# Optimization experiments

Measured on AMD Instinct MI355X. Metric: run time of the kernel, lower is better.

Reference implementation:

```python
import jax, jax.numpy as jnp
import numpy as np

MEL = 80  # seq2seq_dim


def gru_step(x, h, Wg, bg, Wc, bc):
    """TF GRUCell: gates=[r,u], new_h = u*h + (1-u)*c."""
    gates = jax.nn.sigmoid(jnp.concatenate([x, h], axis=-1) @ Wg + bg)
    r, u = jnp.split(gates, 2, axis=-1)
    c = jnp.tanh(jnp.concatenate([x, r * h], axis=-1) @ Wc + bc)
    return u * h + (1.0 - u) * c


def setup_inputs() -> dict:
    key = jax.random.key(0)
    B, T_enc, D_enc = 128, 1024, 256
    n_styles, style_dim = 10, 256
    reduc, T_dec = 5, 250
    ks = jax.random.split(key, 20)
    rn = lambda k, shape, s=0.05: jax.random.normal(k, shape, jnp.float32) * s
    return {
        "encoder_output": rn(ks[0], (B, T_enc, D_enc), 1.0),
        "inp_mask": jax.random.randint(ks[1], (B,), 1, T_enc + 1, dtype=jnp.int32),
        "inp_att": jax.nn.softmax(rn(ks[2], (B, n_styles), 1.0), axis=-1),
        "style_token": rn(ks[3], (n_styles, style_dim)),
        # decoder prenet 80->256->128
        "pre_W1": rn(ks[4], (MEL, 256)), "pre_b1": jnp.zeros((256,), jnp.float32),
        "pre_W2": rn(ks[5], (256, 128)), "pre_b2": jnp.zeros((128,), jnp.float32),
        # attention GRU cell: input = [context(256), prenet(128)] = 384, hidden 256
        "att_Wg": rn(ks[6], (384 + 256, 512)), "att_bg": jnp.ones((512,), jnp.float32),
        "att_Wc": rn(ks[7], (384 + 256, 256)), "att_bc": jnp.zeros((256,), jnp.float32),
        # Bahdanau attention (depth 256)
        "attn_Wk": rn(ks[8], (256, 256)), "attn_bk": jnp.zeros((256,), jnp.float32),
        "attn_Wq": rn(ks[9], (256, 256)), "attn_bq": jnp.zeros((256,), jnp.float32),
        "attn_v": rn(ks[10], (256,)),
        # dec_input dense: [att_out(256), weighting_context(256)] -> 256
        "deci_W": rn(ks[11], (512, 256)), "deci_b": jnp.zeros((256,), jnp.float32),
        # two residual GRU decoder layers (hidden 256)
        "dec1_Wg": rn(ks[12], (512, 512)), "dec1_bg": jnp.ones((512,), jnp.float32),
        "dec1_Wc": rn(ks[13], (512, 256)), "dec1_bc": jnp.zeros((256,), jnp.float32),
        "dec2_Wg": rn(ks[14], (512, 512)), "dec2_bg": jnp.ones((512,), jnp.float32),
        "dec2_Wc": rn(ks[15], (512, 256)), "dec2_bc": jnp.zeros((256,), jnp.float32),
        # output projection 256 -> mel*reduc
        "out_W": rn(ks[16], (256, MEL * reduc)), "out_b": jnp.zeros((MEL * reduc,), jnp.float32),
        "decode_time_steps": T_dec,
    }


def reference(encoder_output, inp_mask, inp_att, style_token,
              pre_W1, pre_b1, pre_W2, pre_b2,
              att_Wg, att_bg, att_Wc, att_bc,
              attn_Wk, attn_bk, attn_Wq, attn_bq, attn_v,
              deci_W, deci_b,
              dec1_Wg, dec1_bg, dec1_Wc, dec1_bc,
              dec2_Wg, dec2_bg, dec2_Wc, dec2_bc,
              out_W, out_b, decode_time_steps):
    B, T_enc, D = encoder_output.shape
    reduc = out_W.shape[1] // MEL
    # precompute attention keys and mask (done once in TF AttentionModule)
    keys = encoder_output @ attn_Wk + attn_bk                       # [B, T_enc, 256]
    mask = jnp.arange(T_enc)[None, :] < inp_mask[:, None]           # [B, T_enc]
    sentence_style = inp_att @ style_token                          # [B, 256]
    abs_style = jnp.abs(sentence_style)

    carry0 = (
        jnp.zeros((B, 256), jnp.float32),   # att GRU state
        jnp.zeros((B, 256), jnp.float32),   # dec GRU layer 1 state
        jnp.zeros((B, 256), jnp.float32),   # dec GRU layer 2 state
        jnp.zeros((B, 256), jnp.float32),   # last context
        jnp.zeros((B, MEL), jnp.float32),   # go frame / last output
    )

    def step(carry, _):
        h_att, h1, h2, ctx, last_out = carry
        # decoder prenet (dropout inactive, training=False)
        p = jax.nn.relu(last_out @ pre_W1 + pre_b1)
        p = jax.nn.relu(p @ pre_W2 + pre_b2)
        # attention RNN
        h_att = gru_step(jnp.concatenate([ctx, p], axis=-1), h_att,
                         att_Wg, att_bg, att_Wc, att_bc)
        # Bahdanau attention with query = attention cell state
        q = h_att @ attn_Wq + attn_bq                               # [B, 256]
        e = jnp.einsum('btd,d->bt', jnp.tanh(keys + q[:, None, :]), attn_v)
        e = jnp.where(mask, e, -1e9)
        alpha = jax.nn.softmax(e, axis=-1)                          # [B, T_enc]
        context = jnp.einsum('bt,btd->bd', alpha, encoder_output)   # [B, 256]
        # style-weighted context
        wctx = context + sentence_style
        weight_per = jnp.mean(abs_style / (jnp.abs(context) + abs_style))
        # decoder RNN: dense then 2 residual GRU layers
        dec_in = jnp.concatenate([h_att, wctx], axis=-1) @ deci_W + deci_b
        h1 = gru_step(dec_in, h1, dec1_Wg, dec1_bg, dec1_Wc, dec1_bc)
        o1 = h1 + dec_in
        h2 = gru_step(o1, h2, dec2_Wg, dec2_bg, dec2_Wc, dec2_bc)
        o2 = h2 + o1
        dense_out = o2 @ out_W + out_b                              # [B, mel*reduc]
        new_out = dense_out[:, -MEL:]
        return (h_att, h1, h2, context, new_out), (dense_out, alpha, weight_per)

    _, (dense_outs, alphas, weight_pers) = jax.lax.scan(
        step, carry0, None, length=decode_time_steps)
    # [T_dec, B, mel*reduc] -> [B, T_dec*reduc, mel]
    seq2seq_output = jnp.transpose(dense_outs, (1, 0, 2)).reshape(
        B, decode_time_steps * reduc, MEL)
    return seq2seq_output, alphas, weight_pers
```

## Files before the change

kernel.cpp:

```cpp
#include <hip/hip_runtime.h>
#include <cstdint>
#include <cstddef>


#define TDEC   250
#define BATCH  128

#define ALPHA_OFF  ((size_t)12800000)
#define WP_OFF     ((size_t)45568000)

#define WS_WACC_B   ((size_t)0)
#define WS_WGT_B    ((size_t)4096)
#define WGT_ELEMS   1658880
#define WS_KEYS_B   (WS_WGT_B + (size_t)WGT_ELEMS * 2)
#define WS_ENC_B    (WS_KEYS_B + (size_t)33554432 * 2)

#define OFF_PRE_W1   0
#define OFF_PRE_W2   20480
#define OFF_ATT_WG   53248
#define OFF_ATT_WC   380928
#define OFF_ATT_WCH  479232
#define OFF_ATTN_WQ  544768
#define OFF_DECI_W   610304
#define OFF_DEC1_WG  741376
#define OFF_DEC1_WC  1003520
#define OFF_DEC1_WCH 1069056
#define OFF_DEC2_WG  1134592
#define OFF_DEC2_WC  1396736
#define OFF_DEC2_WCH 1462272
#define OFF_OUT_WP   1527808

__device__ inline float bf2f(unsigned short u){
    return __uint_as_float(((unsigned int)u) << 16);
}
__device__ inline unsigned short f2bf(float f){
    unsigned int u = __float_as_uint(f);
    u = (u + 0x7fffu + ((u >> 16) & 1u)) >> 16;
    return (unsigned short)u;
}
__device__ inline float ftanh(float x){
    float e = __expf(2.f * x);
    return 1.f - 2.f * __builtin_amdgcn_rcpf(e + 1.f);
}
__device__ inline float fsig(float x){
    return __builtin_amdgcn_rcpf(1.f + __expf(-x));
}

template<int K, int N, int PARTS>
__device__ inline void gemv_part(const unsigned short* __restrict__ W,
                                 const float* __restrict__ x,
                                 float* __restrict__ scratch, int tid)
{
    constexpr int CH   = N / 8;
    constexpr int LG   = (CH == 16) ? 4 : (CH == 32) ? 5 : 6;
    constexpr int KCNT = K / PARTS;
    static_assert(KCNT * PARTS == K, "K must divide");
    static_assert(CH * PARTS <= 1024, "too many threads");
    const int chunk = tid & (CH - 1);
    const int part  = tid >> LG;
    if (PARTS == (1024 >> LG) || part < PARTS){
        const uint4* Wp = (const uint4*)W + (size_t)(part * KCNT) * (N / 8) + chunk;
        const float* xp = x + part * KCNT;
        float a0=0.f,a1=0.f,a2=0.f,a3=0.f,a4=0.f,a5=0.f,a6=0.f,a7=0.f;
        #pragma unroll 8
        for (int k = 0; k < KCNT; k++){
            uint4 w = Wp[(size_t)k * (N / 8)];
            float xv = xp[k];
            a0 = fmaf(__uint_as_float(w.x << 16),         xv, a0);
            a1 = fmaf(__uint_as_float(w.x & 0xffff0000u), xv, a1);
            a2 = fmaf(__uint_as_float(w.y << 16),         xv, a2);
            a3 = fmaf(__uint_as_float(w.y & 0xffff0000u), xv, a3);
            a4 = fmaf(__uint_as_float(w.z << 16),         xv, a4);
            a5 = fmaf(__uint_as_float(w.z & 0xffff0000u), xv, a5);
            a6 = fmaf(__uint_as_float(w.w << 16),         xv, a6);
            a7 = fmaf(__uint_as_float(w.w & 0xffff0000u), xv, a7);
        }
        float4* s4 = (float4*)(scratch + part * N + chunk * 8);
        s4[0] = float4{a0, a1, a2, a3};
        s4[1] = float4{a4, a5, a6, a7};
    }
}

template<int N, int PARTS>
__device__ inline float red_parts(const float* __restrict__ scratch, int n){
    float s = 0.f;
    #pragma unroll
    for (int p = 0; p < PARTS; p++) s += scratch[p * N + n];
    return s;
}

__global__ void k_cvt_flat(const float* __restrict__ src, unsigned short* __restrict__ dst, int n){
    int i = blockIdx.x * 256 + threadIdx.x;
    if (i < n) dst[i] = f2bf(src[i]);
}
__global__ void k_cvt_pad(const float* __restrict__ src, unsigned short* __restrict__ dst){
    int i = blockIdx.x * 256 + threadIdx.x;
    int k = i >> 9, n = i & 511;
    dst[i] = (n < 400) ? f2bf(src[k * 400 + n]) : (unsigned short)0;
}

__global__ __launch_bounds__(256) void k_keys(const float* __restrict__ enc,
                                              const float* __restrict__ Wk,
                                              const float* __restrict__ bk,
                                              unsigned short* __restrict__ keysT)
{
    __shared__ __align__(16) float Wt[64 * 256];
    __shared__ float At[64 * 64];
    __shared__ unsigned short tileT[256 * 68];
    const int tid = threadIdx.x;
    const size_t row0 = (size_t)blockIdx.x * 64;
    const int dq = tid & 63;
    const int rg = tid >> 6;

    float4 acc[16];
    #pragma unroll
    for (int i = 0; i < 16; i++) acc[i] = float4{0.f, 0.f, 0.f, 0.f};

    for (int k0 = 0; k0 < 256; k0 += 64){
        __syncthreads();
        #pragma unroll
        for (int i = 0; i < 64; i++)
            Wt[i * 256 + tid] = Wk[(size_t)(k0 + i) * 256 + tid];
        #pragma unroll
        for (int i = 0; i < 16; i++){
            int idx = tid + i * 256;
            int r = idx >> 6, kk = idx & 63;
            At[idx] = enc[(row0 + r) * 256 + k0 + kk];
        }
        __syncthreads();
        for (int kk = 0; kk < 64; kk++){
            float4 w = ((const float4*)Wt)[kk * 64 + dq];
            #pragma unroll
            for (int rr = 0; rr < 16; rr++){
                float a = At[(rg * 16 + rr) * 64 + kk];
                acc[rr].x += a * w.x; acc[rr].y += a * w.y;
                acc[rr].z += a * w.z; acc[rr].w += a * w.w;
            }
        }
    }
    float4 bb = ((const float4*)bk)[dq];
    __syncthreads();
    #pragma unroll
    for (int rr = 0; rr < 16; rr++){
        int t_loc = rg * 16 + rr;
        #pragma unroll
        for (int c = 0; c < 4; c++){
            float val = (&acc[rr].x)[c] + (&bb.x)[c];
            int d = dq * 4 + c;
            tileT[d * 68 + t_loc] = f2bf(val);
        }
    }
    __syncthreads();
    const int b_ = (int)(row0 >> 10);
    const int t0 = (int)(row0 & 1023);
    #pragma unroll
    for (int i = 0; i < 16; i++){
        int flat = tid + i * 256;
        int d = flat >> 4, tq = flat & 15;
        ushort4 v = *(const ushort4*)&tileT[d * 68 + tq * 4];
        *(ushort4*)&keysT[(((size_t)(b_ * 256 + d)) << 10) + t0 + tq * 4] = v;
    }
}

struct KParams {
    const int *imask; const float *inp_att; const float *style_tok;
    const float *pre_b1, *pre_b2, *att_bg, *att_bc, *attn_bq, *attn_v;
    const float *deci_b, *dec1_bg, *dec1_bc, *dec2_bg, *dec2_bc, *out_b;
    const unsigned short *wgt;
    const unsigned short *keysT;
    const unsigned short *encb;
    float *wacc; float *out;
};

__global__ __launch_bounds__(1024, 1) void k_main(KParams p)
{
    __shared__ __align__(16) float scr [8192];
    __shared__ __align__(16) float scr2[8192];
    __shared__ float xa[640];
    __shared__ float xg[512];
    __shared__ float xr[256];
    __shared__ float xd[512];
    __shared__ float g_l[512], cx_l[256];
    __shared__ float h_att[256], h1[256], h2[256];
    __shared__ float p1_l[256], dci[256], o1_l[256], o2_l[256];
    __shared__ float stylel[256], astylel[256], v_l[256], q_l[256];
    __shared__ float e_l[1024];
    __shared__ float last_o[80];
    __shared__ float red[16];

    const int tid = threadIdx.x;
    const int b   = blockIdx.x;
    const int mlen = p.imask[b];
    const unsigned short* W = p.wgt;

    if (tid < 256){
        h_att[tid] = 0.f; h1[tid] = 0.f; h2[tid] = 0.f;
        float s = 0.f;
        #pragma unroll
        for (int k = 0; k < 10; k++) s += p.inp_att[b * 10 + k] * p.style_tok[k * 256 + tid];
        stylel[tid] = s; astylel[tid] = fabsf(s);
        v_l[tid] = p.attn_v[tid];
        xa[tid] = 0.f;
        xa[384 + tid] = 0.f;
    }
    if (tid < 80) last_o[tid] = 0.f;
    __syncthreads();

    for (int s = 0; s < TDEC; s++){
        gemv_part<80, 256, 16>(W + OFF_PRE_W1, last_o, scr, tid);
        __syncthreads();
        if (tid < 256)
            p1_l[tid] = fmaxf(p.pre_b1[tid] + red_parts<256,16>(scr, tid), 0.f);
        __syncthreads();

        gemv_part<256, 128, 64>(W + OFF_PRE_W2, p1_l, scr, tid);
        __syncthreads();
        if (tid < 128)
            xa[256 + tid] = fmaxf(p.pre_b2[tid] + red_parts<128,64>(scr, tid), 0.f);
        __syncthreads();

        gemv_part<640, 512, 16>(W + OFF_ATT_WG, xa, scr,  tid);
        gemv_part<384, 256, 32>(W + OFF_ATT_WC, xa, scr2, tid);
        __syncthreads();
        if (tid < 512){
            float g = fsig(p.att_bg[tid] + red_parts<512,16>(scr, tid));
            g_l[tid] = g;
            if (tid < 256) xr[tid] = g * h_att[tid];
        } else if (tid < 768){
            int n = tid - 512;
            cx_l[n] = p.att_bc[n] + red_parts<256,32>(scr2, n);
        }
        __syncthreads();

        gemv_part<256, 256, 32>(W + OFF_ATT_WCH, xr, scr, tid);
        __syncthreads();
        if (tid < 256){
            float c = ftanh(cx_l[tid] + red_parts<256,32>(scr, tid));
            float u = g_l[256 + tid];
            float h = u * h_att[tid] + (1.f - u) * c;
            h_att[tid] = h;
            xa[384 + tid] = h;
            xd[tid] = h;
        }
        __syncthreads();

        gemv_part<256, 256, 32>(W + OFF_ATTN_WQ, h_att, scr, tid);
        __syncthreads();
        if (tid < 256) q_l[tid] = p.attn_bq[tid] + red_parts<256,32>(scr, tid);
        __syncthreads();

        {
            const int tc   = tid & 127;
            const int part = tid >> 7;
            float acc0=0.f,acc1=0.f,acc2=0.f,acc3=0.f,acc4=0.f,acc5=0.f,acc6=0.f,acc7=0.f;
            if (tc * 8 < mlen){
                const unsigned short* kp = p.keysT + (((size_t)b) << 18)
                                         + ((size_t)(part * 32) << 10) + tc * 8;
                #pragma unroll 16
                for (int dd = 0; dd < 32; dd++){
                    uint4 kv = *(const uint4*)(kp + ((size_t)dd << 10));
                    int d = part * 32 + dd;
                    float qd = q_l[d], vd = v_l[d];
                    acc0 = fmaf(ftanh(__uint_as_float(kv.x << 16)         + qd), vd, acc0);
                    acc1 = fmaf(ftanh(__uint_as_float(kv.x & 0xffff0000u) + qd), vd, acc1);
                    acc2 = fmaf(ftanh(__uint_as_float(kv.y << 16)         + qd), vd, acc2);
                    acc3 = fmaf(ftanh(__uint_as_float(kv.y & 0xffff0000u) + qd), vd, acc3);
                    acc4 = fmaf(ftanh(__uint_as_float(kv.z << 16)         + qd), vd, acc4);
                    acc5 = fmaf(ftanh(__uint_as_float(kv.z & 0xffff0000u) + qd), vd, acc5);
                    acc6 = fmaf(ftanh(__uint_as_float(kv.w << 16)         + qd), vd, acc6);
                    acc7 = fmaf(ftanh(__uint_as_float(kv.w & 0xffff0000u) + qd), vd, acc7);
                }
            }
            float4* s4 = (float4*)(scr + part * 1024 + tc * 8);
            s4[0] = float4{acc0, acc1, acc2, acc3};
            s4[1] = float4{acc4, acc5, acc6, acc7};
        }
        __syncthreads();
        float av = 0.f;
        if (tid < mlen){
            float s8 = 0.f;
            #pragma unroll
            for (int pp = 0; pp < 8; pp++) s8 += scr[pp * 1024 + tid];
            av = __expf(s8);
        }
        {
            float ws = av;
            #pragma unroll
            for (int off = 32; off; off >>= 1) ws += __shfl_xor(ws, off, 64);
            if ((tid & 63) == 0) red[tid >> 6] = ws;
        }
        __syncthreads();
        {
            float tot = 0.f;
            #pragma unroll
            for (int i = 0; i < 16; i++) tot += red[i];
            float alpha = av * __builtin_amdgcn_rcpf(tot);
            e_l[tid] = alpha;
            __builtin_nontemporal_store(alpha,
                &p.out[ALPHA_OFF + (size_t)s * 131072 + ((size_t)b << 10) + tid]);
        }
        __syncthreads();

        {
            const int dc = tid & 31;
            const int tp = tid >> 5;
            float acc0=0.f,acc1=0.f,acc2=0.f,acc3=0.f,acc4=0.f,acc5=0.f,acc6=0.f,acc7=0.f;
            const unsigned short* er = p.encb + (((size_t)b) << 18) + dc * 8;
            #pragma unroll 8
            for (int t = tp; t < mlen; t += 32){
                uint4 ev4 = *(const uint4*)(er + ((size_t)t << 8));
                float al = e_l[t];
                acc0 = fmaf(al, __uint_as_float(ev4.x << 16),         acc0);
                acc1 = fmaf(al, __uint_as_float(ev4.x & 0xffff0000u), acc1);
                acc2 = fmaf(al, __uint_as_float(ev4.y << 16),         acc2);
                acc3 = fmaf(al, __uint_as_float(ev4.y & 0xffff0000u), acc3);
                acc4 = fmaf(al, __uint_as_float(ev4.z << 16),         acc4);
                acc5 = fmaf(al, __uint_as_float(ev4.z & 0xffff0000u), acc5);
                acc6 = fmaf(al, __uint_as_float(ev4.w << 16),         acc6);
                acc7 = fmaf(al, __uint_as_float(ev4.w & 0xffff0000u), acc7);
            }
            float4* s4 = (float4*)(scr + tp * 256 + dc * 8);
            s4[0] = float4{acc0, acc1, acc2, acc3};
            s4[1] = float4{acc4, acc5, acc6, acc7};
        }
        __syncthreads();
        if (tid < 256){
            float cs = red_parts<256,32>(scr, tid);
            xa[tid] = cs;
            xd[256 + tid] = cs + stylel[tid];
            float wpv = astylel[tid] * __builtin_amdgcn_rcpf(fabsf(cs) + astylel[tid]);
            #pragma unroll
            for (int off = 32; off; off >>= 1) wpv += __shfl_xor(wpv, off, 64);
            if ((tid & 63) == 0) atomicAdd(&p.wacc[s], wpv);
        }
        __syncthreads();

        gemv_part<512, 256, 32>(W + OFF_DECI_W, xd, scr, tid);
        __syncthreads();
        if (tid < 256){
            float d = p.deci_b[tid] + red_parts<256,32>(scr, tid);
            dci[tid] = d;
            xg[tid] = d; xg[256 + tid] = h1[tid];
        }
        __syncthreads();

        gemv_part<512, 512, 16>(W + OFF_DEC1_WG, xg, scr,  tid);
        gemv_part<256, 256, 32>(W + OFF_DEC1_WC, xg, scr2, tid);
        __syncthreads();
        if (tid < 512){
            float g = fsig(p.dec1_bg[tid] + red_parts<512,16>(scr, tid));
            g_l[tid] = g;
            if (tid < 256) xr[tid] = g * h1[tid];
        } else if (tid < 768){
            int n = tid - 512;
            cx_l[n] = p.dec1_bc[n] + red_parts<256,32>(scr2, n);
        }
        __syncthreads();

        gemv_part<256, 256, 32>(W + OFF_DEC1_WCH, xr, scr, tid);
        __syncthreads();
        if (tid < 256){
            float c = ftanh(cx_l[tid] + red_parts<256,32>(scr, tid));
            float u = g_l[256 + tid];
            float hn = u * h1[tid] + (1.f - u) * c;
            h1[tid] = hn;
            float o1 = hn + dci[tid];
            o1_l[tid] = o1;
            xg[tid] = o1; xg[256 + tid] = h2[tid];
        }
        __syncthreads();

        gemv_part<512, 512, 16>(W + OFF_DEC2_WG, xg, scr,  tid);
        gemv_part<256, 256, 32>(W + OFF_DEC2_WC, xg, scr2, tid);
        __syncthreads();
        if (tid < 512){
            float g = fsig(p.dec2_bg[tid] + red_parts<512,16>(scr, tid));
            g_l[tid] = g;
            if (tid < 256) xr[tid] = g * h2[tid];
        } else if (tid < 768){
            int n = tid - 512;
            cx_l[n] = p.dec2_bc[n] + red_parts<256,32>(scr2, n);
        }
        __syncthreads();

        gemv_part<256, 256, 32>(W + OFF_DEC2_WCH, xr, scr, tid);
        __syncthreads();
        if (tid < 256){
            float c = ftanh(cx_l[tid] + red_parts<256,32>(scr, tid));
            float u = g_l[256 + tid];
            float hn = u * h2[tid] + (1.f - u) * c;
            h2[tid] = hn;
            o2_l[tid] = hn + o1_l[tid];
        }
        __syncthreads();

        gemv_part<256, 512, 16>(W + OFF_OUT_WP, o2_l, scr, tid);
        __syncthreads();
        if (tid < 400){
            float val = p.out_b[tid] + red_parts<512,16>(scr, tid);
            __builtin_nontemporal_store(val,
                &p.out[(size_t)b * 100000 + (size_t)s * 400 + tid]);
            if (tid >= 320) last_o[tid - 320] = val;
        }
        __syncthreads();
    }
}

__global__ void k_final(const float* __restrict__ wacc, float* __restrict__ out)
{
    int i = threadIdx.x;
    if (i < TDEC) out[WP_OFF + i] = wacc[i] * (1.0f / 32768.0f);
}

extern "C" void kernel_launch(void* const* d_in, const int* in_sizes, int n_in,
                              void* d_out, int out_size, void* d_ws, size_t ws_size,
                              hipStream_t stream)
{
    const float* enc        = (const float*)d_in[0];
    const int*   imask      = (const int*)  d_in[1];
    const float* inp_att    = (const float*)d_in[2];
    const float* style_tok  = (const float*)d_in[3];
    const float* pre_W1     = (const float*)d_in[4];
    const float* pre_b1     = (const float*)d_in[5];
    const float* pre_W2     = (const float*)d_in[6];
    const float* pre_b2     = (const float*)d_in[7];
    const float* att_Wg     = (const float*)d_in[8];
    const float* att_bg     = (const float*)d_in[9];
    const float* att_Wc     = (const float*)d_in[10];
    const float* att_bc     = (const float*)d_in[11];
    const float* attn_Wk    = (const float*)d_in[12];
    const float* attn_bk    = (const float*)d_in[13];
    const float* attn_Wq    = (const float*)d_in[14];
    const float* attn_bq    = (const float*)d_in[15];
    const float* attn_v     = (const float*)d_in[16];
    const float* deci_W     = (const float*)d_in[17];
    const float* deci_b     = (const float*)d_in[18];
    const float* dec1_Wg    = (const float*)d_in[19];
    const float* dec1_bg    = (const float*)d_in[20];
    const float* dec1_Wc    = (const float*)d_in[21];
    const float* dec1_bc    = (const float*)d_in[22];
    const float* dec2_Wg    = (const float*)d_in[23];
    const float* dec2_bg    = (const float*)d_in[24];
    const float* dec2_Wc    = (const float*)d_in[25];
    const float* dec2_bc    = (const float*)d_in[26];
    const float* out_W      = (const float*)d_in[27];
    const float* out_b      = (const float*)d_in[28];

    float*          wacc  = (float*)((char*)d_ws + WS_WACC_B);
    unsigned short* wgt   = (unsigned short*)((char*)d_ws + WS_WGT_B);
    unsigned short* keysT = (unsigned short*)((char*)d_ws + WS_KEYS_B);
    unsigned short* encb  = (unsigned short*)((char*)d_ws + WS_ENC_B);
    float* out = (float*)d_out;

    hipMemsetAsync(d_ws, 0, 1024, stream);

    auto cvt = [&](const float* src, size_t off, int n){
        k_cvt_flat<<<(n + 255) / 256, 256, 0, stream>>>(src, wgt + off, n);
    };
    cvt(pre_W1,  OFF_PRE_W1,   80 * 256);
    cvt(pre_W2,  OFF_PRE_W2,  256 * 128);
    cvt(att_Wg,  OFF_ATT_WG,  640 * 512);
    cvt(att_Wc,  OFF_ATT_WC,  640 * 256);
    cvt(attn_Wq, OFF_ATTN_WQ, 256 * 256);
    cvt(deci_W,  OFF_DECI_W,  512 * 256);
    cvt(dec1_Wg, OFF_DEC1_WG, 512 * 512);
    cvt(dec1_Wc, OFF_DEC1_WC, 512 * 256);
    cvt(dec2_Wg, OFF_DEC2_WG, 512 * 512);
    cvt(dec2_Wc, OFF_DEC2_WC, 512 * 256);
    k_cvt_pad<<<(256 * 512) / 256, 256, 0, stream>>>(out_W, wgt + OFF_OUT_WP);

    k_cvt_flat<<<(33554432 + 255) / 256, 256, 0, stream>>>(enc, encb, 33554432);

    k_keys<<<2048, 256, 0, stream>>>(enc, attn_Wk, attn_bk, keysT);

    KParams kp{imask, inp_att, style_tok,
               pre_b1, pre_b2, att_bg, att_bc, attn_bq, attn_v,
               deci_b, dec1_bg, dec1_bc, dec2_bg, dec2_bc, out_b,
               wgt, keysT, encb, wacc, out};
    k_main<<<BATCH, 1024, 0, stream>>>(kp);

    k_final<<<1, 256, 0, stream>>>(wacc, out);
}
```

Measured before the change: 23.70 ms.

## Switch decoder GEMVs to fp16 dot2 with k-interleaved weight layout

Weights are stored in fp16 with an 8-wide k-interleaved layout so each thread owns one output column and consumes 8 k-elements per 16-byte load using v_dot2 instructions. Activations feeding the GEMVs are kept in fp16 shared buffers, and the k-split shrinks from 16–64 parts to 2–8, so the cross-part reductions after each GEMV get much cheaper. The aim is to cut ALU and LDS reduction work in the latency-bound per-step recurrent loop. Precision changes from bf16 to fp16 weights and fp16 activations, which adds overflow and accuracy risk.

```diff
diff --git a/kernel.cpp b/kernel.cpp
--- a/kernel.cpp
+++ b/kernel.cpp
@@ -30,9 +30,10 @@
 #define OFF_DEC2_WCH 1462272
 #define OFF_OUT_WP   1527808
 
-__device__ inline float bf2f(unsigned short u){
-    return __uint_as_float(((unsigned int)u) << 16);
-}
+typedef _Float16 f16;
+typedef f16 f16x2 __attribute__((ext_vector_type(2)));
+typedef f16 f16x8 __attribute__((ext_vector_type(8)));
+
 __device__ inline unsigned short f2bf(float f){
     unsigned int u = __float_as_uint(f);
     u = (u + 0x7fffu + ((u >> 16) & 1u)) >> 16;
@@ -46,57 +47,54 @@
     return __builtin_amdgcn_rcpf(1.f + __expf(-x));
 }
 
+__device__ inline float fdot2f(f16x2 a, f16x2 b, float c){
+#if __has_builtin(__builtin_amdgcn_fdot2)
+    return __builtin_amdgcn_fdot2(a, b, c, false);
+#else
+    return c + (float)a.x * (float)b.x + (float)a.y * (float)b.y;
+#endif
+}
+
 template<int K, int N, int PARTS>
-__device__ inline void gemv_part(const unsigned short* __restrict__ W,
-                                 const float* __restrict__ x,
-                                 float* __restrict__ scratch, int tid)
+__device__ inline void gemv_dot(const f16* __restrict__ W,
+                                const f16* __restrict__ xh,
+                                float* __restrict__ scratch, int tid)
 {
-    constexpr int CH   = N / 8;
-    constexpr int LG   = (CH == 16) ? 4 : (CH == 32) ? 5 : 6;
-    constexpr int KCNT = K / PARTS;
-    static_assert(KCNT * PARTS == K, "K must divide");
-    static_assert(CH * PARTS <= 1024, "too many threads");
-    const int chunk = tid & (CH - 1);
-    const int part  = tid >> LG;
-    if (PARTS == (1024 >> LG) || part < PARTS){
-        const uint4* Wp = (const uint4*)W + (size_t)(part * KCNT) * (N / 8) + chunk;
-        const float* xp = x + part * KCNT;
-        float a0=0.f,a1=0.f,a2=0.f,a3=0.f,a4=0.f,a5=0.f,a6=0.f,a7=0.f;
-        #pragma unroll 8
-        for (int k = 0; k < KCNT; k++){
-            uint4 w = Wp[(size_t)k * (N / 8)];
-            float xv = xp[k];
-            a0 = fmaf(__uint_as_float(w.x << 16),         xv, a0);
-            a1 = fmaf(__uint_as_float(w.x & 0xffff0000u), xv, a1);
-            a2 = fmaf(__uint_as_float(w.y << 16),         xv, a2);
-            a3 = fmaf(__uint_as_float(w.y & 0xffff0000u), xv, a3);
-            a4 = fmaf(__uint_as_float(w.z << 16),         xv, a4);
-            a5 = fmaf(__uint_as_float(w.z & 0xffff0000u), xv, a5);
-            a6 = fmaf(__uint_as_float(w.w << 16),         xv, a6);
-            a7 = fmaf(__uint_as_float(w.w & 0xffff0000u), xv, a7);
-        }
-        float4* s4 = (float4*)(scratch + part * N + chunk * 8);
-        s4[0] = float4{a0, a1, a2, a3};
-        s4[1] = float4{a4, a5, a6, a7};
+    constexpr int LGN = (N == 128) ? 7 : (N == 256) ? 8 : 9;
+    constexpr int NT  = K / (8 * PARTS);
+    static_assert(NT * 8 * PARTS == K, "K must split into 8-elem tiles");
+    static_assert(N * PARTS <= 1024, "too many threads");
+    const int n    = tid & (N - 1);
+    const int part = tid >> LGN;
+    if (PARTS == (1024 >> LGN) || part < PARTS){
+        const f16x8* Wp = (const f16x8*)W + (size_t)(part * NT) * N + n;
+        const f16x8* xp = (const f16x8*)xh + part * NT;
+        float acc = 0.f;
+        #pragma unroll
+        for (int t = 0; t < NT; t++){
+            union { f16x8 v; f16x2 p[4]; } w, xv;
+            w.v  = Wp[(size_t)t * N];
+            xv.v = xp[t];
+            acc = fdot2f(w.p[0], xv.p[0], acc);
+            acc = fdot2f(w.p[1], xv.p[1], acc);
+            acc = fdot2f(w.p[2], xv.p[2], acc);
+            acc = fdot2f(w.p[3], xv.p[3], acc);
+        }
+        scratch[part * N + n] = acc;
     }
-}
-
-template<int N, int PARTS>
-__device__ inline float red_parts(const float* __restrict__ scratch, int n){
-    float s = 0.f;
-    #pragma unroll
-    for (int p = 0; p < PARTS; p++) s += scratch[p * N + n];
-    return s;
 }
 
 __global__ void k_cvt_flat(const float* __restrict__ src, unsigned short* __restrict__ dst, int n){
     int i = blockIdx.x * 256 + threadIdx.x;
     if (i < n) dst[i] = f2bf(src[i]);
 }
-__global__ void k_cvt_pad(const float* __restrict__ src, unsigned short* __restrict__ dst){
+__global__ void k_cvt_dot(const float* __restrict__ src, f16* __restrict__ dst,
+                          int K, int N, int srcN, int row0){
     int i = blockIdx.x * 256 + threadIdx.x;
-    int k = i >> 9, n = i & 511;
-    dst[i] = (n < 400) ? f2bf(src[k * 400 + n]) : (unsigned short)0;
+    if (i >= K * N) return;
+    int k = i / N, n = i - k * N;
+    float v = (n < srcN) ? src[(size_t)(row0 + k) * srcN + n] : 0.f;
+    dst[((size_t)(k >> 3) * N + n) * 8 + (k & 7)] = (f16)v;
 }
 
 __global__ __launch_bounds__(256) void k_keys(const float* __restrict__ enc,
@@ -166,7 +164,7 @@
     const int *imask; const float *inp_att; const float *style_tok;
     const float *pre_b1, *pre_b2, *att_bg, *att_bc, *attn_bq, *attn_v;
     const float *deci_b, *dec1_bg, *dec1_bc, *dec2_bg, *dec2_bc, *out_b;
-    const unsigned short *wgt;
+    const f16 *wgt;
     const unsigned short *keysT;
     const unsigned short *encb;
     float *wacc; float *out;
@@ -175,23 +173,25 @@
 __global__ __launch_bounds__(1024, 1) void k_main(KParams p)
 {
     __shared__ __align__(16) float scr [8192];
-    __shared__ __align__(16) float scr2[8192];
-    __shared__ float xa[640];
-    __shared__ float xg[512];
-    __shared__ float xr[256];
-    __shared__ float xd[512];
+    __shared__ __align__(16) float scr2[2048];
+    __shared__ float e_l[1024];
     __shared__ float g_l[512], cx_l[256];
-    __shared__ float h_att[256], h1[256], h2[256];
-    __shared__ float p1_l[256], dci[256], o1_l[256], o2_l[256];
+    __shared__ float h_att[256], h1[256], h2[256], dci[256], o1_l[256];
     __shared__ float stylel[256], astylel[256], v_l[256], q_l[256];
-    __shared__ float e_l[1024];
-    __shared__ float last_o[80];
     __shared__ float red[16];
+    __shared__ __align__(16) f16 xah[640];
+    __shared__ __align__(16) f16 xdh[512];
+    __shared__ __align__(16) f16 xgh[512];
+    __shared__ __align__(16) f16 xrh[256];
+    __shared__ __align__(16) f16 xr2h[256];
+    __shared__ __align__(16) f16 o2h[256];
+    __shared__ __align__(16) f16 p1h[256];
+    __shared__ __align__(16) f16 lastoh[80];
 
     const int tid = threadIdx.x;
     const int b   = blockIdx.x;
     const int mlen = p.imask[b];
-    const unsigned short* W = p.wgt;
+    const f16* W = p.wgt;
 
     if (tid < 256){
         h_att[tid] = 0.f; h1[tid] = 0.f; h2[tid] = 0.f;
@@ -200,53 +200,68 @@
         for (int k = 0; k < 10; k++) s += p.inp_att[b * 10 + k] * p.style_tok[k * 256 + tid];
         stylel[tid] = s; astylel[tid] = fabsf(s);
         v_l[tid] = p.attn_v[tid];
-        xa[tid] = 0.f;
-        xa[384 + tid] = 0.f;
+        xah[tid] = (f16)0.f;
+        xah[384 + tid] = (f16)0.f;
     }
-    if (tid < 80) last_o[tid] = 0.f;
+    if (tid < 80) lastoh[tid] = (f16)0.f;
     __syncthreads();
 
     for (int s = 0; s < TDEC; s++){
-        gemv_part<80, 256, 16>(W + OFF_PRE_W1, last_o, scr, tid);
+        gemv_dot<80, 256, 2>(W + OFF_PRE_W1, lastoh, scr2, tid);
         __syncthreads();
         if (tid < 256)
-            p1_l[tid] = fmaxf(p.pre_b1[tid] + red_parts<256,16>(scr, tid), 0.f);
-        __syncthreads();
-
-        gemv_part<256, 128, 64>(W + OFF_PRE_W2, p1_l, scr, tid);
-        __syncthreads();
-        if (tid < 128)
-            xa[256 + tid] = fmaxf(p.pre_b2[tid] + red_parts<128,64>(scr, tid), 0.f);
-        __syncthreads();
-
-        gemv_part<640, 512, 16>(W + OFF_ATT_WG, xa, scr,  tid);
-        gemv_part<384, 256, 32>(W + OFF_ATT_WC, xa, scr2, tid);
+            p1h[tid] = (f16)fmaxf(p.pre_b1[tid] + scr2[tid] + scr2[256 + tid], 0.f);
+        __syncthreads();
+
+        gemv_dot<256, 128, 8>(W + OFF_PRE_W2, p1h, scr2, tid);
+        __syncthreads();
+        if (tid < 128){
+            float sv = p.pre_b2[tid];
+            #pragma unroll
+            for (int q = 0; q < 8; q++) sv += scr2[q * 128 + tid];
+            xah[256 + tid] = (f16)fmaxf(sv, 0.f);
+        }
+        __syncthreads();
+
+        gemv_dot<640, 512, 2>(W + OFF_ATT_WG, xah, scr,  tid);
+        gemv_dot<384, 256, 4>(W + OFF_ATT_WC, xah, scr2, tid);
         __syncthreads();
         if (tid < 512){
-            float g = fsig(p.att_bg[tid] + red_parts<512,16>(scr, tid));
+            float g = fsig(p.att_bg[tid] + scr[tid] + scr[512 + tid]);
             g_l[tid] = g;
-            if (tid < 256) xr[tid] = g * h_att[tid];
+            if (tid < 256) xrh[tid] = (f16)(g * h_att[tid]);
         } else if (tid < 768){
             int n = tid - 512;
-            cx_l[n] = p.att_bc[n] + red_parts<256,32>(scr2, n);
-        }
-        __syncthreads();
-
-        gemv_part<256, 256, 32>(W + OFF_ATT_WCH, xr, scr, tid);
+            float sv = p.att_bc[n];
+            #pragma unroll
+            for (int q = 0; q < 4; q++) sv += scr2[q * 256 + n];
+            cx_l[n] = sv;
+        }
+        __syncthreads();
+
+        gemv_dot<256, 256, 4>(W + OFF_ATT_WCH, xrh, scr2, tid);
         __syncthreads();
         if (tid < 256){
-            float c = ftanh(cx_l[tid] + red_parts<256,32>(scr, tid));
+            float sv = cx_l[tid];
+            #pragma unroll
+            for (int q = 0; q < 4; q++) sv += scr2[q * 256 + tid];
+            float c = ftanh(sv);
             float u = g_l[256 + tid];
             float h = u * h_att[tid] + (1.f - u) * c;
             h_att[tid] = h;
-            xa[384 + tid] = h;
-            xd[tid] = h;
-        }
-        __syncthreads();
-
-        gemv_part<256, 256, 32>(W + OFF_ATTN_WQ, h_att, scr, tid);
-        __syncthreads();
-        if (tid < 256) q_l[tid] = p.attn_bq[tid] + red_parts<256,32>(scr, tid);
+            xah[384 + tid] = (f16)h;
+            xdh[tid] = (f16)h;
+        }
+        __syncthreads();
+
+        gemv_dot<256, 256, 4>(W + OFF_ATTN_WQ, xah + 384, scr2, tid);
+        __syncthreads();
+        if (tid < 256){
+            float sv = p.attn_bq[tid];
+            #pragma unroll
+            for (int q = 0; q < 4; q++) sv += scr2[q * 256 + tid];
+            q_l[tid] = sv;
+        }
         __syncthreads();
 
         {
@@ -325,9 +340,11 @@
         }
         __syncthreads();
         if (tid < 256){
-            float cs = red_parts<256,32>(scr, tid);
-            xa[tid] = cs;
-            xd[256 + tid] = cs + stylel[tid];
+            float cs = 0.f;
+            #pragma unroll
+            for (int pp = 0; pp < 32; pp++) cs += scr[pp * 256 + tid];
+            xah[tid] = (f16)cs;
+            xdh[256 + tid] = (f16)(cs + stylel[tid]);
             float wpv = astylel[tid] * __builtin_amdgcn_rcpf(fabsf(cs) + astylel[tid]);
             #pragma unroll
             for (int off = 32; off; off >>= 1) wpv += __shfl_xor(wpv, off, 64);
@@ -335,72 +352,86 @@
         }
         __syncthreads();
 
-        gemv_part<512, 256, 32>(W + OFF_DECI_W, xd, scr, tid);
+        gemv_dot<512, 256, 4>(W + OFF_DECI_W, xdh, scr2, tid);
         __syncthreads();
         if (tid < 256){
-            float d = p.deci_b[tid] + red_parts<256,32>(scr, tid);
-            dci[tid] = d;
-            xg[tid] = d; xg[256 + tid] = h1[tid];
-        }
-        __syncthreads();
-
-        gemv_part<512, 512, 16>(W + OFF_DEC1_WG, xg, scr,  tid);
-        gemv_part<256, 256, 32>(W + OFF_DEC1_WC, xg, scr2, tid);
+            float sv = p.deci_b[tid];
+            #pragma unroll
+            for (int q = 0; q < 4; q++) sv += scr2[q * 256 + tid];
+            dci[tid] = sv;
+            xgh[tid] = (f16)sv; xgh[256 + tid] = (f16)h1[tid];
+        }
+        __syncthreads();
+
+        gemv_dot<512, 512, 2>(W + OFF_DEC1_WG, xgh, scr,  tid);
+        gemv_dot<256, 256, 4>(W + OFF_DEC1_WC, xgh, scr2, tid);
         __syncthreads();
         if (tid < 512){
-            float g = fsig(p.dec1_bg[tid] + red_parts<512,16>(scr, tid));
+            float g = fsig(p.dec1_bg[tid] + scr[tid] + scr[512 + tid]);
             g_l[tid] = g;
-            if (tid < 256) xr[tid] = g * h1[tid];
+            if (tid < 256) xr2h[tid] = (f16)(g * h1[tid]);
         } else if (tid < 768){
             int n = tid - 512;
-            cx_l[n] = p.dec1_bc[n] + red_parts<256,32>(scr2, n);
-        }
-        __syncthreads();
-
-        gemv_part<256, 256, 32>(W + OFF_DEC1_WCH, xr, scr, tid);
+            float sv = p.dec1_bc[n];
+            #pragma unroll
+            for (int q = 0; q < 4; q++) sv += scr2[q * 256 + n];
+            cx_l[n] = sv;
+        }
+        __syncthreads();
+
+        gemv_dot<256, 256, 4>(W + OFF_DEC1_WCH, xr2h, scr2, tid);
         __syncthreads();
         if (tid < 256){
-            float c = ftanh(cx_l[tid] + red_parts<256,32>(scr, tid));
+            float sv = cx_l[tid];
+            #pragma unroll
+            for (int q = 0; q < 4; q++) sv += scr2[q * 256 + tid];
+            float c = ftanh(sv);
             float u = g_l[256 + tid];
             float hn = u * h1[tid] + (1.f - u) * c;
             h1[tid] = hn;
             float o1 = hn + dci[tid];
             o1_l[tid] = o1;
-            xg[tid] = o1; xg[256 + tid] = h2[tid];
-        }
-        __syncthreads();
-
-        gemv_part<512, 512, 16>(W + OFF_DEC2_WG, xg, scr,  tid);
-        gemv_part<256, 256, 32>(W + OFF_DEC2_WC, xg, scr2, tid);
+            xgh[tid] = (f16)o1; xgh[256 + tid] = (f16)h2[tid];
+        }
+        __syncthreads();
+
+        gemv_dot<512, 512, 2>(W + OFF_DEC2_WG, xgh, scr,  tid);
+        gemv_dot<256, 256, 4>(W + OFF_DEC2_WC, xgh, scr2, tid);
         __syncthreads();
         if (tid < 512){
-            float g = fsig(p.dec2_bg[tid] + red_parts<512,16>(scr, tid));
+            float g = fsig(p.dec2_bg[tid] + scr[tid] + scr[512 + tid]);
             g_l[tid] = g;
-            if (tid < 256) xr[tid] = g * h2[tid];
+            if (tid < 256) xr2h[tid] = (f16)(g * h2[tid]);
         } else if (tid < 768){
             int n = tid - 512;
-            cx_l[n] = p.dec2_bc[n] + red_parts<256,32>(scr2, n);
-        }
-        __syncthreads();
-
-        gemv_part<256, 256, 32>(W + OFF_DEC2_WCH, xr, scr, tid);
+            float sv = p.dec2_bc[n];
+            #pragma unroll
+            for (int q = 0; q < 4; q++) sv += scr2[q * 256 + n];
+            cx_l[n] = sv;
+        }
+        __syncthreads();
+
+        gemv_dot<256, 256, 4>(W + OFF_DEC2_WCH, xr2h, scr2, tid);
         __syncthreads();
         if (tid < 256){
-            float c = ftanh(cx_l[tid] + red_parts<256,32>(scr, tid));
+            float sv = cx_l[tid];
+            #pragma unroll
+            for (int q = 0; q < 4; q++) sv += scr2[q * 256 + tid];
+            float c = ftanh(sv);
             float u = g_l[256 + tid];
             float hn = u * h2[tid] + (1.f - u) * c;
             h2[tid] = hn;
-            o2_l[tid] = hn + o1_l[tid];
-        }
-        __syncthreads();
-
-        gemv_part<256, 512, 16>(W + OFF_OUT_WP, o2_l, scr, tid);
+            o2h[tid] = (f16)(hn + o1_l[tid]);
+        }
+        __syncthreads();
+
+        gemv_dot<256, 512, 2>(W + OFF_OUT_WP, o2h, scr, tid);
         __syncthreads();
         if (tid < 400){
-            float val = p.out_b[tid] + red_parts<512,16>(scr, tid);
+            float val = p.out_b[tid] + scr[tid] + scr[512 + tid];
             __builtin_nontemporal_store(val,
                 &p.out[(size_t)b * 100000 + (size_t)s * 400 + tid]);
-            if (tid >= 320) last_o[tid - 320] = val;
+            if (tid >= 320) lastoh[tid - 320] = (f16)val;
         }
         __syncthreads();
     }
@@ -447,27 +478,30 @@
     const float* out_b      = (const float*)d_in[28];
 
     float*          wacc  = (float*)((char*)d_ws + WS_WACC_B);
-    unsigned short* wgt   = (unsigned short*)((char*)d_ws + WS_WGT_B);
+    f16*            wgt   = (f16*)  ((char*)d_ws + WS_WGT_B);
     unsigned short* keysT = (unsigned short*)((char*)d_ws + WS_KEYS_B);
     unsigned short* encb  = (unsigned short*)((char*)d_ws + WS_ENC_B);
     float* out = (float*)d_out;
 
     hipMemsetAsync(d_ws, 0, 1024, stream);
 
-    auto cvt = [&](const float* src, size_t off, int n){
-        k_cvt_flat<<<(n + 255) / 256, 256, 0, stream>>>(src, wgt + off, n);
+    auto cvtd = [&](const float* src, size_t off, int K, int N, int srcN, int row0){
+        k_cvt_dot<<<(K * N + 255) / 256, 256, 0, stream>>>(src, wgt + off, K, N, srcN, row0);
     };
-    cvt(pre_W1,  OFF_PRE_W1,   80 * 256);
-    cvt(pre_W2,  OFF_PRE_W2,  256 * 128);
-    cvt(att_Wg,  OFF_ATT_WG,  640 * 512);
-    cvt(att_Wc,  OFF_ATT_WC,  640 * 256);
-    cvt(attn_Wq, OFF_ATTN_WQ, 256 * 256);
-    cvt(deci_W,  OFF_DECI_W,  512 * 256);
-    cvt(dec1_Wg, OFF_DEC1_WG, 512 * 512);
-    cvt(dec1_Wc, OFF_DEC1_WC, 512 * 256);
-    cvt(dec2_Wg, OFF_DEC2_WG, 512 * 512);
-    cvt(dec2_Wc, OFF_DEC2_WC, 512 * 256);
-    k_cvt_pad<<<(256 * 512) / 256, 256, 0, stream>>>(out_W, wgt + OFF_OUT_WP);
+    cvtd(pre_W1,  OFF_PRE_W1,    80, 256, 256, 0);
+    cvtd(pre_W2,  OFF_PRE_W2,   256, 128, 128, 0);
+    cvtd(att_Wg,  OFF_ATT_WG,   640, 512, 512, 0);
+    cvtd(att_Wc,  OFF_ATT_WC,   384, 256, 256, 0);
+    cvtd(att_Wc,  OFF_ATT_WCH,  256, 256, 256, 384);
+    cvtd(attn_Wq, OFF_ATTN_WQ,  256, 256, 256, 0);
+    cvtd(deci_W,  OFF_DECI_W,   512, 256, 256, 0);
+    cvtd(dec1_Wg, OFF_DEC1_WG,  512, 512, 512, 0);
+    cvtd(dec1_Wc, OFF_DEC1_WC,  256, 256, 256, 0);
+    cvtd(dec1_Wc, OFF_DEC1_WCH, 256, 256, 256, 256);
+    cvtd(dec2_Wg, OFF_DEC2_WG,  512, 512, 512, 0);
+    cvtd(dec2_Wc, OFF_DEC2_WC,  256, 256, 256, 0);
+    cvtd(dec2_Wc, OFF_DEC2_WCH, 256, 256, 256, 256);
+    cvtd(out_W,   OFF_OUT_WP,   256, 512, 400, 0);
 
     k_cvt_flat<<<(33554432 + 255) / 256, 256, 0, stream>>>(enc, encb, 33554432);
 
```

New measurement: 45.28 ms. 1.91x slower.

## Store GEMV weights as fp16 and add short-sequence attention score path

Applied to the files above, without the earlier changes.

Weight matrices are now converted to fp16 instead of bf16, and the GEMV reads them as fp16 vectors and converts them in hardware. The change is mainly meant to tighten numerics, since the bandwidth stays the same. For batch rows whose mask length is at most 512, the attention score loop now spreads the first 512 positions over 16 parts of 16 depth dims each. This uses all 1024 threads and skips work on masked-out positions. The reduction adapts to the new layout, and fp16 brings range limits on the weights.

```diff
diff --git a/kernel.cpp b/kernel.cpp
--- a/kernel.cpp
+++ b/kernel.cpp
@@ -30,9 +30,9 @@
 #define OFF_DEC2_WCH 1462272
 #define OFF_OUT_WP   1527808
 
-__device__ inline float bf2f(unsigned short u){
-    return __uint_as_float(((unsigned int)u) << 16);
-}
+typedef _Float16 f16;
+typedef f16 f16x8 __attribute__((ext_vector_type(8)));
+
 __device__ inline unsigned short f2bf(float f){
     unsigned int u = __float_as_uint(f);
     u = (u + 0x7fffu + ((u >> 16) & 1u)) >> 16;
@@ -47,7 +47,7 @@
 }
 
 template<int K, int N, int PARTS>
-__device__ inline void gemv_part(const unsigned short* __restrict__ W,
+__device__ inline void gemv_part(const f16* __restrict__ W,
                                  const float* __restrict__ x,
                                  float* __restrict__ scratch, int tid)
 {
@@ -59,21 +59,21 @@
     const int chunk = tid & (CH - 1);
     const int part  = tid >> LG;
     if (PARTS == (1024 >> LG) || part < PARTS){
-        const uint4* Wp = (const uint4*)W + (size_t)(part * KCNT) * (N / 8) + chunk;
+        const f16x8* Wp = (const f16x8*)W + (size_t)(part * KCNT) * (N / 8) + chunk;
         const float* xp = x + part * KCNT;
         float a0=0.f,a1=0.f,a2=0.f,a3=0.f,a4=0.f,a5=0.f,a6=0.f,a7=0.f;
         #pragma unroll 8
         for (int k = 0; k < KCNT; k++){
-            uint4 w = Wp[(size_t)k * (N / 8)];
+            f16x8 w = Wp[(size_t)k * (N / 8)];
             float xv = xp[k];
-            a0 = fmaf(__uint_as_float(w.x << 16),         xv, a0);
-            a1 = fmaf(__uint_as_float(w.x & 0xffff0000u), xv, a1);
-            a2 = fmaf(__uint_as_float(w.y << 16),         xv, a2);
-            a3 = fmaf(__uint_as_float(w.y & 0xffff0000u), xv, a3);
-            a4 = fmaf(__uint_as_float(w.z << 16),         xv, a4);
-            a5 = fmaf(__uint_as_float(w.z & 0xffff0000u), xv, a5);
-            a6 = fmaf(__uint_as_float(w.w << 16),         xv, a6);
-            a7 = fmaf(__uint_as_float(w.w & 0xffff0000u), xv, a7);
+            a0 = fmaf((float)w[0], xv, a0);
+            a1 = fmaf((float)w[1], xv, a1);
+            a2 = fmaf((float)w[2], xv, a2);
+            a3 = fmaf((float)w[3], xv, a3);
+            a4 = fmaf((float)w[4], xv, a4);
+            a5 = fmaf((float)w[5], xv, a5);
+            a6 = fmaf((float)w[6], xv, a6);
+            a7 = fmaf((float)w[7], xv, a7);
         }
         float4* s4 = (float4*)(scratch + part * N + chunk * 8);
         s4[0] = float4{a0, a1, a2, a3};
@@ -93,10 +93,14 @@
     int i = blockIdx.x * 256 + threadIdx.x;
     if (i < n) dst[i] = f2bf(src[i]);
 }
-__global__ void k_cvt_pad(const float* __restrict__ src, unsigned short* __restrict__ dst){
+__global__ void k_cvt_flat16(const float* __restrict__ src, f16* __restrict__ dst, int n){
+    int i = blockIdx.x * 256 + threadIdx.x;
+    if (i < n) dst[i] = (f16)src[i];
+}
+__global__ void k_cvt_pad16(const float* __restrict__ src, f16* __restrict__ dst){
     int i = blockIdx.x * 256 + threadIdx.x;
     int k = i >> 9, n = i & 511;
-    dst[i] = (n < 400) ? f2bf(src[k * 400 + n]) : (unsigned short)0;
+    dst[i] = (n < 400) ? (f16)src[k * 400 + n] : (f16)0.f;
 }
 
 __global__ __launch_bounds__(256) void k_keys(const float* __restrict__ enc,
@@ -166,7 +170,7 @@
     const int *imask; const float *inp_att; const float *style_tok;
     const float *pre_b1, *pre_b2, *att_bg, *att_bc, *attn_bq, *attn_v;
     const float *deci_b, *dec1_bg, *dec1_bc, *dec2_bg, *dec2_bc, *out_b;
-    const unsigned short *wgt;
+    const f16 *wgt;
     const unsigned short *keysT;
     const unsigned short *encb;
     float *wacc; float *out;
@@ -191,7 +195,7 @@
     const int tid = threadIdx.x;
     const int b   = blockIdx.x;
     const int mlen = p.imask[b];
-    const unsigned short* W = p.wgt;
+    const f16* W = p.wgt;
 
     if (tid < 256){
         h_att[tid] = 0.f; h1[tid] = 0.f; h2[tid] = 0.f;
@@ -206,6 +210,8 @@
     if (tid < 80) last_o[tid] = 0.f;
     __syncthreads();
 
+    const bool msmall = (mlen <= 512);
+
     for (int s = 0; s < TDEC; s++){
         gemv_part<80, 256, 16>(W + OFF_PRE_W1, last_o, scr, tid);
         __syncthreads();
@@ -249,7 +255,32 @@
         if (tid < 256) q_l[tid] = p.attn_bq[tid] + red_parts<256,32>(scr, tid);
         __syncthreads();
 
-        {
+        if (msmall){
+            const int tc   = tid & 63;
+            const int part = tid >> 6;
+            float acc0=0.f,acc1=0.f,acc2=0.f,acc3=0.f,acc4=0.f,acc5=0.f,acc6=0.f,acc7=0.f;
+            if (tc * 8 < mlen){
+                const unsigned short* kp = p.keysT + (((size_t)b) << 18)
+                                         + ((size_t)(part * 16) << 10) + tc * 8;
+                #pragma unroll 16
+                for (int dd = 0; dd < 16; dd++){
+                    uint4 kv = *(const uint4*)(kp + ((size_t)dd << 10));
+                    int d = part * 16 + dd;
+                    float qd = q_l[d], vd = v_l[d];
+                    acc0 = fmaf(ftanh(__uint_as_float(kv.x << 16)         + qd), vd, acc0);
+                    acc1 = fmaf(ftanh(__uint_as_float(kv.x & 0xffff0000u) + qd), vd, acc1);
+                    acc2 = fmaf(ftanh(__uint_as_float(kv.y << 16)         + qd), vd, acc2);
+                    acc3 = fmaf(ftanh(__uint_as_float(kv.y & 0xffff0000u) + qd), vd, acc3);
+                    acc4 = fmaf(ftanh(__uint_as_float(kv.z << 16)         + qd), vd, acc4);
+                    acc5 = fmaf(ftanh(__uint_as_float(kv.z & 0xffff0000u) + qd), vd, acc5);
+                    acc6 = fmaf(ftanh(__uint_as_float(kv.w << 16)         + qd), vd, acc6);
+                    acc7 = fmaf(ftanh(__uint_as_float(kv.w & 0xffff0000u) + qd), vd, acc7);
+                }
+            }
+            float4* s4 = (float4*)(scr + part * 512 + tc * 8);
+            s4[0] = float4{acc0, acc1, acc2, acc3};
+            s4[1] = float4{acc4, acc5, acc6, acc7};
+        } else {
             const int tc   = tid & 127;
             const int part = tid >> 7;
             float acc0=0.f,acc1=0.f,acc2=0.f,acc3=0.f,acc4=0.f,acc5=0.f,acc6=0.f,acc7=0.f;
@@ -279,8 +310,13 @@
         float av = 0.f;
         if (tid < mlen){
             float s8 = 0.f;
-            #pragma unroll
-            for (int pp = 0; pp < 8; pp++) s8 += scr[pp * 1024 + tid];
+            if (msmall){
+                #pragma unroll
+                for (int pp = 0; pp < 16; pp++) s8 += scr[pp * 512 + tid];
+            } else {
+                #pragma unroll
+                for (int pp = 0; pp < 8; pp++) s8 += scr[pp * 1024 + tid];
+            }
             av = __expf(s8);
         }
         {
@@ -447,7 +483,7 @@
     const float* out_b      = (const float*)d_in[28];
 
     float*          wacc  = (float*)((char*)d_ws + WS_WACC_B);
-    unsigned short* wgt   = (unsigned short*)((char*)d_ws + WS_WGT_B);
+    f16*            wgt   = (f16*)  ((char*)d_ws + WS_WGT_B);
     unsigned short* keysT = (unsigned short*)((char*)d_ws + WS_KEYS_B);
     unsigned short* encb  = (unsigned short*)((char*)d_ws + WS_ENC_B);
     float* out = (float*)d_out;
@@ -455,7 +491,7 @@
     hipMemsetAsync(d_ws, 0, 1024, stream);
 
     auto cvt = [&](const float* src, size_t off, int n){
-        k_cvt_flat<<<(n + 255) / 256, 256, 0, stream>>>(src, wgt + off, n);
+        k_cvt_flat16<<<(n + 255) / 256, 256, 0, stream>>>(src, wgt + off, n);
     };
     cvt(pre_W1,  OFF_PRE_W1,   80 * 256);
     cvt(pre_W2,  OFF_PRE_W2,  256 * 128);
@@ -467,7 +503,7 @@
     cvt(dec1_Wc, OFF_DEC1_WC, 512 * 256);
     cvt(dec2_Wg, OFF_DEC2_WG, 512 * 512);
     cvt(dec2_Wc, OFF_DEC2_WC, 512 * 256);
-    k_cvt_pad<<<(256 * 512) / 256, 256, 0, stream>>>(out_W, wgt + OFF_OUT_WP);
+    k_cvt_pad16<<<(256 * 512) / 256, 256, 0, stream>>>(out_W, wgt + OFF_OUT_WP);
 
     k_cvt_flat<<<(33554432 + 255) / 256, 256, 0, stream>>>(enc, encb, 33554432);
 
```

After: 21.11 ms. -10.9%, faster.
